# Kernel tuning notes

Hardware: AMD Instinct MI355X
Metric: run time of the kernel (lower is better)

## Reference

```python
import jax, jax.numpy as jnp
import numpy as np

B, S, H = 2, 2048, 2048
NH, NKV = 16, 4
HD = H // NH           # 128
THETA = 1000000.0


def setup_inputs() -> dict:
    key = jax.random.key(0)
    ks = jax.random.split(key, 6)
    s = 0.02
    hidden_states = jax.random.normal(ks[0], (B, S, H), jnp.float32)
    # additive causal mask, broadcast over batch and heads
    causal = jnp.tril(jnp.ones((S, S), bool))
    attention_mask = jnp.where(causal, 0.0, -1e9).astype(jnp.float32)[None, None]
    position_ids = jnp.broadcast_to(jnp.arange(S, dtype=jnp.int32), (B, S))
    wq = jax.random.normal(ks[1], (H, H), jnp.float32) * s
    bq = jnp.zeros((H,), jnp.float32)
    wk = jax.random.normal(ks[2], (H, NKV * HD), jnp.float32) * s
    bk = jnp.zeros((NKV * HD,), jnp.float32)
    wv = jax.random.normal(ks[3], (H, NKV * HD), jnp.float32) * s
    bv = jnp.zeros((NKV * HD,), jnp.float32)
    wo = jax.random.normal(ks[4], (H, H), jnp.float32) * s
    return {"hidden_states": hidden_states, "attention_mask": attention_mask,
            "position_ids": position_ids, "wq": wq, "bq": bq, "wk": wk, "bk": bk,
            "wv": wv, "bv": bv, "wo": wo}


def _rope(x, cos, sin):
    # x: [B,S,h,HD]; interleaved-pair rotation == complex multiply in original
    x2 = x.reshape(*x.shape[:-1], HD // 2, 2)
    x0, x1 = x2[..., 0], x2[..., 1]
    r0 = x0 * cos - x1 * sin
    r1 = x0 * sin + x1 * cos
    return jnp.stack([r0, r1], axis=-1).reshape(x.shape).astype(jnp.float32)


def reference(hidden_states, attention_mask, position_ids, wq, bq, wk, bk, wv, bv, wo):
    bf = jnp.bfloat16
    x = hidden_states.astype(bf)
    # projections in bf16, as flax Dense(dtype=bfloat16)
    q = (x @ wq.astype(bf) + bq.astype(bf)).reshape(B, S, NH, HD)
    k = (x @ wk.astype(bf) + bk.astype(bf)).reshape(B, S, NKV, HD)
    v = (x @ wv.astype(bf) + bv.astype(bf)).reshape(B, S, NKV, HD)
    # RoPE: freqs_cis = exp(1j * pos * inv_freq); real rotation form, identical math
    pos = position_ids[0].astype(jnp.float32)                       # [S]
    inv = 1.0 / (THETA ** (jnp.arange(0, HD, 2, dtype=jnp.float32) / HD))  # [HD/2]
    ang = pos[:, None] * inv[None, :]                               # [S, HD/2]
    cos = jnp.cos(ang)[None, :, None, :]
    sin = jnp.sin(ang)[None, :, None, :]
    q = _rope(q, cos, sin)   # cast to float32 per module dtype
    k = _rope(k, cos, sin)
    cache_k, cache_v = k, v.astype(jnp.float32)
    rep = NH // NKV
    kr = jnp.repeat(k, rep, axis=2)                                 # [B,S,NH,HD]
    vr = jnp.repeat(v, rep, axis=2).astype(jnp.float32)
    scale = 1.0 / np.sqrt(HD).astype(np.float32)
    scores = jnp.einsum('bqhd,bkhd->bhqk', q, kr) * scale + attention_mask
    # float64 cast in original is a no-op w/o x64; softmax runs in float32
    probs = jnp.clip(jax.nn.softmax(scores, axis=-1), 1e-9, 1.0 - 1e-9)
    attn = jnp.einsum('bhqk,bkhd->bqhd', probs, vr).reshape(B, S, H)
    out = attn.astype(bf) @ wo.astype(bf)   # o_proj, no bias, bf16
    return out, (cache_k, cache_v)
```

## Files before the change

kernel.cpp:

```cpp
#include <hip/hip_runtime.h>
#include <hip/hip_bf16.h>
#include <math.h>

#define B_    2
#define S_    2048
#define H_    2048
#define NH_   16
#define NKV_  4
#define HD_   128
#define M_    (B_*S_)
#define NKVH_ (NKV_*HD_)
#define QKVN  3072
#define PSTR  72

typedef __bf16 bf16x8 __attribute__((ext_vector_type(8)));
typedef __bf16 bf16x4 __attribute__((ext_vector_type(4)));
typedef float  f32x4  __attribute__((ext_vector_type(4)));

__device__ __forceinline__ float bf2f(unsigned short u){
  unsigned int i = ((unsigned int)u) << 16; float f;
  __builtin_memcpy(&f, &i, 4); return f;
}
__device__ __forceinline__ unsigned short f2bf(float f){
  unsigned int i; __builtin_memcpy(&i, &f, 4);
  unsigned int r = (i + 0x7fffu + ((i >> 16) & 1u)) >> 16;
  return (unsigned short)r;
}
__device__ __forceinline__ float fast_exp2(float x){
  float r; asm("v_exp_f32 %0, %1" : "=v"(r) : "v"(x)); return r;
}

#define GLOAD_LDS16(g, l) __builtin_amdgcn_global_load_lds( \
    (const __attribute__((address_space(1))) void*)(g), \
    (__attribute__((address_space(3))) void*)(l), 16, 0, 0)

__global__ void k_f32_to_bf16(const float* __restrict__ in, unsigned short* __restrict__ out, int n4){
  int idx = blockIdx.x * blockDim.x + threadIdx.x;
  if (idx >= n4) return;
  float4 v = reinterpret_cast<const float4*>(in)[idx];
  ushort4 o; o.x = f2bf(v.x); o.y = f2bf(v.y); o.z = f2bf(v.z); o.w = f2bf(v.w);
  reinterpret_cast<ushort4*>(out)[idx] = o;
}

__global__ void k_transpose_w(const float* __restrict__ W, unsigned short* __restrict__ Wt, int K, int N){
  __shared__ unsigned short tile[32][36];
  int t = threadIdx.x;
  int k0 = blockIdx.x * 32, n0 = blockIdx.y * 32;
  int kr = t >> 3, nc = (t & 7) * 4;
  float4 v = *reinterpret_cast<const float4*>(&W[(size_t)(k0 + kr) * N + n0 + nc]);
  tile[kr][nc+0] = f2bf(v.x); tile[kr][nc+1] = f2bf(v.y);
  tile[kr][nc+2] = f2bf(v.z); tile[kr][nc+3] = f2bf(v.w);
  __syncthreads();
  int nr = t >> 3, kc = (t & 7) * 4;
  ushort4 o;
  o.x = tile[kc+0][nr]; o.y = tile[kc+1][nr]; o.z = tile[kc+2][nr]; o.w = tile[kc+3][nr];
  *reinterpret_cast<ushort4*>(&Wt[(size_t)(n0 + nr) * K + k0 + kc]) = o;
}

__global__ void k_bias_cat(const float* __restrict__ bq, const float* __restrict__ bk,
                           const float* __restrict__ bv, float* __restrict__ out){
  int i = blockIdx.x * 256 + threadIdx.x;
  if (i >= QKVN) return;
  out[i] = (i < H_) ? bq[i] : (i < H_ + NKVH_ ? bk[i - H_] : bv[i - H_ - NKVH_]);
}

__global__ void k_rope_table(const int* __restrict__ pos, float2* __restrict__ tab){
  int idx = blockIdx.x * blockDim.x + threadIdx.x;
  if (idx >= S_ * 64) return;
  int s = idx >> 6, i = idx & 63;
  float p = (float)pos[s];
  float inv = expf(-(float)i * (13.815510557964274f / 64.0f));
  float ang = p * inv;
  tab[idx] = make_float2(cosf(ang), sinf(ang));
}

__global__ void k_rope_k(unsigned short* __restrict__ QKV, const float2* __restrict__ tab,
                         float* __restrict__ cacheK){
  int idx = blockIdx.x * blockDim.x + threadIdx.x;
  int row = idx >> 7;
  int col0 = (idx & 127) * 4;
  int s = row & (S_ - 1);
  int i0 = (col0 & (HD_ - 1)) >> 1;
  unsigned short* p = QKV + (size_t)row * QKVN + H_ + col0;
  ushort4 v = *reinterpret_cast<ushort4*>(p);
  float2 t0 = tab[(s << 6) + i0], t1 = tab[(s << 6) + i0 + 1];
  float x0 = bf2f(v.x), x1 = bf2f(v.y), x2 = bf2f(v.z), x3 = bf2f(v.w);
  float r0 = x0 * t0.x - x1 * t0.y;
  float r1 = x0 * t0.y + x1 * t0.x;
  float r2 = x2 * t1.x - x3 * t1.y;
  float r3 = x2 * t1.y + x3 * t1.x;
  ushort4 o; o.x = f2bf(r0); o.y = f2bf(r1); o.z = f2bf(r2); o.w = f2bf(r3);
  *reinterpret_cast<ushort4*>(p) = o;
  float4 c; c.x = r0; c.y = r1; c.z = r2; c.w = r3;
  reinterpret_cast<float4*>(cacheK)[idx] = c;
}

__global__ void k_transpose_v(const unsigned short* __restrict__ QKV, unsigned short* __restrict__ Vt,
                              float* __restrict__ cacheV){
  __shared__ unsigned short tile[32][36];
  int t = threadIdx.x;
  int s0 = blockIdx.x * 32, c0 = blockIdx.y * 32, b = blockIdx.z;
  int sr = t >> 3, cc = (t & 7) * 4;
  ushort4 v = *reinterpret_cast<const ushort4*>(
      &QKV[(size_t)(b * S_ + s0 + sr) * QKVN + H_ + NKVH_ + c0 + cc]);
  tile[sr][cc+0] = v.x; tile[sr][cc+1] = v.y; tile[sr][cc+2] = v.z; tile[sr][cc+3] = v.w;
  float4 cf; cf.x = bf2f(v.x); cf.y = bf2f(v.y); cf.z = bf2f(v.z); cf.w = bf2f(v.w);
  *reinterpret_cast<float4*>(&cacheV[(size_t)(b * S_ + s0 + sr) * NKVH_ + c0 + cc]) = cf;
  __syncthreads();
  int cr = t >> 3, sc = (t & 7) * 4;
  ushort4 o;
  o.x = tile[sc+0][cr]; o.y = tile[sc+1][cr]; o.z = tile[sc+2][cr]; o.w = tile[sc+3][cr];
  *reinterpret_cast<ushort4*>(&Vt[(size_t)(b * NKVH_ + c0 + cr) * S_ + s0 + sc]) = o;
}

__global__ __launch_bounds__(256) void k_gemm_bt(
    const unsigned short* __restrict__ A,
    const unsigned short* __restrict__ Bt,
    const float* __restrict__ bias,
    unsigned short* __restrict__ Cb,
    float* __restrict__ Cf,
    int M, int N, int K)
{
  __shared__ unsigned short As[128 * 32];
  __shared__ unsigned short Bs[128 * 32];
  const int nbn = N >> 7;
  const int bm = blockIdx.x / nbn, bn = blockIdx.x % nbn;
  const int tid = threadIdx.x, lane = tid & 63, wave = tid >> 6;
  const int wr = wave >> 1, wc = wave & 1;
  const int gm0 = bm << 7, gn0 = bn << 7;
  const int l15 = lane & 15, lhi = lane >> 4;
  const int srow = lane >> 2, scol = (lane & 3) * 8;

  f32x4 acc[4][4];
  f32x4 zero = {0.f, 0.f, 0.f, 0.f};
  #pragma unroll
  for (int m = 0; m < 4; m++)
    #pragma unroll
    for (int n = 0; n < 4; n++) acc[m][n] = zero;

  for (int k0 = 0; k0 < K; k0 += 32) {
    __syncthreads();
    #pragma unroll
    for (int it = 0; it < 2; ++it) {
      int c = it * 4 + wave;
      const unsigned short* gA = A + (size_t)(gm0 + c * 16 + srow) * K + k0 + scol;
      GLOAD_LDS16(gA, As + c * 512);
      const unsigned short* gB = Bt + (size_t)(gn0 + c * 16 + srow) * K + k0 + scol;
      GLOAD_LDS16(gB, Bs + c * 512);
    }
    __syncthreads();
    bf16x8 af[4], bfr[4];
    #pragma unroll
    for (int m = 0; m < 4; m++)
      af[m] = *reinterpret_cast<const bf16x8*>(&As[(wr * 64 + m * 16 + l15) * 32 + lhi * 8]);
    #pragma unroll
    for (int n = 0; n < 4; n++)
      bfr[n] = *reinterpret_cast<const bf16x8*>(&Bs[(wc * 64 + n * 16 + l15) * 32 + lhi * 8]);
    #pragma unroll
    for (int m = 0; m < 4; m++)
      #pragma unroll
      for (int n = 0; n < 4; n++)
        acc[m][n] = __builtin_amdgcn_mfma_f32_16x16x32_bf16(af[m], bfr[n], acc[m][n], 0, 0, 0);
  }

  #pragma unroll
  for (int m = 0; m < 4; m++) {
    #pragma unroll
    for (int n = 0; n < 4; n++) {
      int col = gn0 + wc * 64 + n * 16 + l15;
      float bv = bias ? bias[col] : 0.0f;
      #pragma unroll
      for (int r = 0; r < 4; r++) {
        int row = gm0 + wr * 64 + m * 16 + lhi * 4 + r;
        size_t idx = (size_t)row * N + col;
        float v = acc[m][n][r] + bv;
        if (Cf) Cf[idx] = bf2f(f2bf(v));
        else    Cb[idx] = f2bf(v);
      }
    }
  }
}

__device__ __forceinline__ bf16x8 rope8(ushort4 a, ushort4 b, const float2* __restrict__ tb, float mul){
  unsigned short u[8];
  float2 c;
  c = tb[0]; { float x0=bf2f(a.x), x1=bf2f(a.y); u[0]=f2bf((x0*c.x-x1*c.y)*mul); u[1]=f2bf((x0*c.y+x1*c.x)*mul); }
  c = tb[1]; { float x0=bf2f(a.z), x1=bf2f(a.w); u[2]=f2bf((x0*c.x-x1*c.y)*mul); u[3]=f2bf((x0*c.y+x1*c.x)*mul); }
  c = tb[2]; { float x0=bf2f(b.x), x1=bf2f(b.y); u[4]=f2bf((x0*c.x-x1*c.y)*mul); u[5]=f2bf((x0*c.y+x1*c.x)*mul); }
  c = tb[3]; { float x0=bf2f(b.z), x1=bf2f(b.w); u[6]=f2bf((x0*c.x-x1*c.y)*mul); u[7]=f2bf((x0*c.y+x1*c.x)*mul); }
  bf16x8 r; __builtin_memcpy(&r, u, 16); return r;
}

__global__ __launch_bounds__(256, 2) void k_attn(
    const unsigned short* __restrict__ QKV,
    const unsigned short* __restrict__ Vt,
    const float2* __restrict__ tab,
    unsigned short* __restrict__ O)
{
  __shared__ unsigned short Ks[2][64 * 128];
  __shared__ unsigned short Vs[128 * 64];
  __shared__ unsigned short Plds[4][32 * PSTR];
  const int qb = blockIdx.x;
  const int h = blockIdx.y, b = blockIdx.z;
  const int tid = threadIdx.x, lane = tid & 63, wave = tid >> 6;
  const int l15 = lane & 15, lhi = lane >> 4;
  const int q0a = qb * 64 + wave * 16;
  const int q0b = (31 - qb) * 64 + wave * 16;
  const int kvh = h >> 2;
  const float scale = 0.08838834764831845f;
  const float LOG2E = 1.4426950408889634f;
  const float SHIFT2 = 23.083120654223414f;

  const unsigned short* Kg = QKV + (size_t)(b * S_) * QKVN + H_ + kvh * HD_;
  const unsigned short* Vg = Vt + (size_t)(b * NKV_ + kvh) * HD_ * S_;

  bf16x8 qfa[4], qfb[4];
  {
    const unsigned short* qa = QKV + (size_t)(b * S_ + q0a + l15) * QKVN + h * HD_ + lhi * 8;
    const unsigned short* qbp = QKV + (size_t)(b * S_ + q0b + l15) * QKVN + h * HD_ + lhi * 8;
    const float2* ta = tab + (size_t)(q0a + l15) * 64;
    const float2* tb = tab + (size_t)(q0b + l15) * 64;
    #pragma unroll
    for (int t = 0; t < 4; t++) {
      int i0 = t * 16 + lhi * 4;
      ushort4 a0 = *reinterpret_cast<const ushort4*>(qa + t * 32);
      ushort4 a1 = *reinterpret_cast<const ushort4*>(qa + t * 32 + 4);
      ushort4 b0 = *reinterpret_cast<const ushort4*>(qbp + t * 32);
      ushort4 b1 = *reinterpret_cast<const ushort4*>(qbp + t * 32 + 4);
      qfa[t] = rope8(a0, a1, ta + i0, scale);
      qfb[t] = rope8(b0, b1, tb + i0, scale);
    }
  }

  f32x4 oa[8], ob[8];
  f32x4 zero = {0.f, 0.f, 0.f, 0.f};
  #pragma unroll
  for (int d = 0; d < 8; d++) { oa[d] = zero; ob[d] = zero; }
  float la = 0.f, lb = 0.f;

  unsigned short* pl = &Plds[wave][0];
  const int ktmax = 31 - qb;
  const int krow = tid >> 4, kch = tid & 15;
  const int vrow = tid >> 3, vch = tid & 7;

  auto STAGE_K = [&](int kt, int bi){
    #pragma unroll
    for (int p = 0; p < 4; p++) {
      int r = p * 16 + krow;
      int cs = kch ^ (r & 7);
      GLOAD_LDS16(Kg + (size_t)(kt * 64 + r) * QKVN + cs * 8, &Ks[bi][(p * 16 + 4 * wave) * 128]);
    }
  };
  auto STAGE_V = [&](int kt){
    #pragma unroll
    for (int p = 0; p < 4; p++) {
      int r = p * 32 + vrow;
      int cs = vch ^ (r & 7);
      GLOAD_LDS16(Vg + (size_t)r * S_ + kt * 64 + cs * 8, &Vs[(p * 32 + 8 * wave) * 64]);
    }
  };

  STAGE_K(0, 0);
  __syncthreads();
  int cur = 0;

  for (int kt = 0; kt <= ktmax; ++kt) {
    STAGE_V(kt);
    if (kt < ktmax) STAGE_K(kt + 1, cur ^ 1);
    const bool doA = (kt <= qb);

    f32x4 sca[4], scb[4];
    #pragma unroll
    for (int c = 0; c < 4; c++) { sca[c] = zero; scb[c] = zero; }
    __builtin_amdgcn_s_setprio(1);
    #pragma unroll
    for (int c = 0; c < 4; c++) {
      int rk = c * 16 + l15;
      #pragma unroll
      for (int t = 0; t < 4; t++) {
        bf16x8 kf = *reinterpret_cast<const bf16x8*>(
            &Ks[cur][rk * 128 + (((t << 2) + lhi) ^ (rk & 7)) * 8]);
        scb[c] = __builtin_amdgcn_mfma_f32_16x16x32_bf16(kf, qfb[t], scb[c], 0, 0, 0);
        if (doA) sca[c] = __builtin_amdgcn_mfma_f32_16x16x32_bf16(kf, qfa[t], sca[c], 0, 0, 0);
      }
    }
    __builtin_amdgcn_s_setprio(0);

    {
      int qiB = q0b + l15;
      float acc = 0.f;
      #pragma unroll
      for (int c = 0; c < 4; c++) {
        float pv[4];
        #pragma unroll
        for (int r = 0; r < 4; r++) {
          int key = kt * 64 + c * 16 + lhi * 4 + r;
          float sv = (key > qiB) ? -1e30f : scb[c][r];
          pv[r] = fast_exp2(fmaf(sv, LOG2E, -SHIFT2));
          acc += pv[r];
        }
        bf16x4 w;
        w[0] = (__bf16)pv[0]; w[1] = (__bf16)pv[1]; w[2] = (__bf16)pv[2]; w[3] = (__bf16)pv[3];
        *reinterpret_cast<bf16x4*>(&pl[(16 + l15) * PSTR + c * 16 + lhi * 4]) = w;
      }
      lb += acc;
    }
    if (doA) {
      int qiA = q0a + l15;
      float acc = 0.f;
      #pragma unroll
      for (int c = 0; c < 4; c++) {
        float pv[4];
        #pragma unroll
        for (int r = 0; r < 4; r++) {
          int key = kt * 64 + c * 16 + lhi * 4 + r;
          float sv = (key > qiA) ? -1e30f : sca[c][r];
          pv[r] = fast_exp2(fmaf(sv, LOG2E, -SHIFT2));
          acc += pv[r];
        }
        bf16x4 w;
        w[0] = (__bf16)pv[0]; w[1] = (__bf16)pv[1]; w[2] = (__bf16)pv[2]; w[3] = (__bf16)pv[3];
        *reinterpret_cast<bf16x4*>(&pl[l15 * PSTR + c * 16 + lhi * 4]) = w;
      }
      la += acc;
    }
    asm volatile("" ::: "memory");
    bf16x8 pfb0 = *reinterpret_cast<const bf16x8*>(&pl[(16 + l15) * PSTR + lhi * 8]);
    bf16x8 pfb1 = *reinterpret_cast<const bf16x8*>(&pl[(16 + l15) * PSTR + 32 + lhi * 8]);
    bf16x8 pfa0 = pfb0, pfa1 = pfb1;
    if (doA) {
      pfa0 = *reinterpret_cast<const bf16x8*>(&pl[l15 * PSTR + lhi * 8]);
      pfa1 = *reinterpret_cast<const bf16x8*>(&pl[l15 * PSTR + 32 + lhi * 8]);
    }
    asm volatile("" ::: "memory");

    __syncthreads();

    __builtin_amdgcn_s_setprio(1);
    #pragma unroll
    for (int d = 0; d < 8; d++) {
      int rv = d * 16 + l15;
      bf16x8 vf0 = *reinterpret_cast<const bf16x8*>(&Vs[rv * 64 + (lhi ^ (rv & 7)) * 8]);
      bf16x8 vf1 = *reinterpret_cast<const bf16x8*>(&Vs[rv * 64 + ((4 + lhi) ^ (rv & 7)) * 8]);
      ob[d] = __builtin_amdgcn_mfma_f32_16x16x32_bf16(pfb0, vf0, ob[d], 0, 0, 0);
      ob[d] = __builtin_amdgcn_mfma_f32_16x16x32_bf16(pfb1, vf1, ob[d], 0, 0, 0);
      if (doA) {
        oa[d] = __builtin_amdgcn_mfma_f32_16x16x32_bf16(pfa0, vf0, oa[d], 0, 0, 0);
        oa[d] = __builtin_amdgcn_mfma_f32_16x16x32_bf16(pfa1, vf1, oa[d], 0, 0, 0);
      }
    }
    __builtin_amdgcn_s_setprio(0);

    __syncthreads();
    cur ^= 1;
  }

  la += __shfl_xor(la, 16); la += __shfl_xor(la, 32);
  lb += __shfl_xor(lb, 16); lb += __shfl_xor(lb, 32);

  #pragma unroll
  for (int r = 0; r < 4; r++) {
    int src = (lane & 48) | (lhi * 4 + r);
    float invA = 1.0f / __shfl(la, src);
    float invB = 1.0f / __shfl(lb, src);
    size_t offA = (size_t)(b * S_ + q0a + lhi * 4 + r) * H_ + h * HD_;
    size_t offB = (size_t)(b * S_ + q0b + lhi * 4 + r) * H_ + h * HD_;
    #pragma unroll
    for (int d = 0; d < 8; d++) {
      O[offA + d * 16 + l15] = f2bf(oa[d][r] * invA);
      O[offB + d * 16 + l15] = f2bf(ob[d][r] * invB);
    }
  }
}

extern "C" void kernel_launch(void* const* d_in, const int* in_sizes, int n_in,
                              void* d_out, int out_size, void* d_ws, size_t ws_size,
                              hipStream_t stream) {
  const float* hidden = (const float*)d_in[0];
  const int*   pos    = (const int*)d_in[2];
  const float* wq     = (const float*)d_in[3];
  const float* bq     = (const float*)d_in[4];
  const float* wk     = (const float*)d_in[5];
  const float* bk     = (const float*)d_in[6];
  const float* wv     = (const float*)d_in[7];
  const float* bv     = (const float*)d_in[8];
  const float* wo     = (const float*)d_in[9];

  float* outF   = (float*)d_out;
  float* cacheK = outF + (size_t)M_ * H_;
  float* cacheV = cacheK + (size_t)M_ * NKVH_;

  char* w = (char*)d_ws;
  unsigned short* Xbf  = (unsigned short*)w; w += (size_t)M_ * H_ * 2;
  unsigned short* WqT  = (unsigned short*)w; w += (size_t)H_ * H_ * 2;
  unsigned short* WkT  = (unsigned short*)w; w += (size_t)NKVH_ * H_ * 2;
  unsigned short* WvT  = (unsigned short*)w; w += (size_t)NKVH_ * H_ * 2;
  unsigned short* WoT  = (unsigned short*)w; w += (size_t)H_ * H_ * 2;
  unsigned short* QKVw = (unsigned short*)w; w += (size_t)M_ * QKVN * 2;
  unsigned short* Vt   = (unsigned short*)w; w += (size_t)M_ * NKVH_ * 2;
  float2*         tab  = (float2*)w;         w += (size_t)S_ * 64 * sizeof(float2);
  float*       biasQKV = (float*)w;          w += QKVN * sizeof(float);
  unsigned short* Ao   = Xbf;

  k_f32_to_bf16<<<(M_ * H_ / 4) / 256, 256, 0, stream>>>(hidden, Xbf, M_ * H_ / 4);
  k_transpose_w<<<dim3(64, 64), 256, 0, stream>>>(wq, WqT, H_, H_);
  k_transpose_w<<<dim3(64, 16), 256, 0, stream>>>(wk, WkT, H_, NKVH_);
  k_transpose_w<<<dim3(64, 16), 256, 0, stream>>>(wv, WvT, H_, NKVH_);
  k_transpose_w<<<dim3(64, 64), 256, 0, stream>>>(wo, WoT, H_, H_);
  k_rope_table<<<(S_ * 64) / 256, 256, 0, stream>>>(pos, tab);
  k_bias_cat<<<(QKVN + 255) / 256, 256, 0, stream>>>(bq, bk, bv, biasQKV);
  k_gemm_bt<<<32 * (QKVN >> 7), 256, 0, stream>>>(Xbf, WqT, biasQKV, QKVw, nullptr, M_, QKVN, H_);
  k_rope_k<<<(M_ * NKVH_ / 4) / 256, 256, 0, stream>>>(QKVw, tab, cacheK);
  k_transpose_v<<<dim3(S_ / 32, NKVH_ / 32, B_), 256, 0, stream>>>(QKVw, Vt, cacheV);
  k_attn<<<dim3(16, NH_, B_), 256, 0, stream>>>(QKVw, Vt, tab, Ao);
  k_gemm_bt<<<32 * 16, 256, 0, stream>>>(Ao, WoT, nullptr, nullptr, outF, M_, H_, H_);
}
```

Before: 241.5 us.

## Rewrite projection GEMM with 256x256 tiles, double-buffered LDS and swizzle

Replaces the 128x128, K=32 GEMM with a 512-thread 256x256 tile kernel using K=64 steps. Global-to-LDS loads for the next K tile are double-buffered and interleaved with the MFMA work. The LDS layout is XOR-swizzled to avoid bank conflicts, and blocks are remapped across XCDs. The aim is higher arithmetic intensity and overlap of loads with compute in both projection GEMMs. The costs are 128KB of LDS and 128 accumulator registers per thread, which limit occupancy, and fewer workgroups (192 and 128), which may underfill the 256 CUs.

```diff
diff --git a/kernel.cpp b/kernel.cpp
--- a/kernel.cpp
+++ b/kernel.cpp
@@ -113,7 +113,7 @@
   *reinterpret_cast<ushort4*>(&Vt[(size_t)(b * NKVH_ + c0 + cr) * S_ + s0 + sc]) = o;
 }
 
-__global__ __launch_bounds__(256) void k_gemm_bt(
+__global__ __launch_bounds__(512, 2) void k_gemm256(
     const unsigned short* __restrict__ A,
     const unsigned short* __restrict__ Bt,
     const float* __restrict__ bias,
@@ -121,59 +121,92 @@
     float* __restrict__ Cf,
     int M, int N, int K)
 {
-  __shared__ unsigned short As[128 * 32];
-  __shared__ unsigned short Bs[128 * 32];
-  const int nbn = N >> 7;
-  const int bm = blockIdx.x / nbn, bn = blockIdx.x % nbn;
+  __shared__ unsigned short As[2][256 * 64];
+  __shared__ unsigned short Bs[2][256 * 64];
+  const int nbn = N >> 8;
+  const int nwg = gridDim.x;
+  int bid = blockIdx.x;
+  if ((nwg & 7) == 0) bid = (bid & 7) * (nwg >> 3) + (bid >> 3);
+  const int bm = bid / nbn, bn = bid % nbn;
   const int tid = threadIdx.x, lane = tid & 63, wave = tid >> 6;
-  const int wr = wave >> 1, wc = wave & 1;
-  const int gm0 = bm << 7, gn0 = bn << 7;
+  const int wm = wave >> 2, wn = wave & 3;
+  const int gm0 = bm << 8, gn0 = bn << 8;
   const int l15 = lane & 15, lhi = lane >> 4;
-  const int srow = lane >> 2, scol = (lane & 3) * 8;
-
-  f32x4 acc[4][4];
+  const int srow = lane >> 3;
+  const int sch  = (lane & 7) ^ srow;
+
+  f32x4 acc[8][4];
   f32x4 zero = {0.f, 0.f, 0.f, 0.f};
   #pragma unroll
-  for (int m = 0; m < 4; m++)
+  for (int m = 0; m < 8; m++)
     #pragma unroll
     for (int n = 0; n < 4; n++) acc[m][n] = zero;
 
-  for (int k0 = 0; k0 < K; k0 += 32) {
+  const int nt = K >> 6;
+
+  auto STAGE_P = [&](int kt, int bi, int p){
+    int row = p * 64 + wave * 8 + srow;
+    GLOAD_LDS16(A  + (size_t)(gm0 + row) * K + kt * 64 + sch * 8,
+                &As[bi][(p * 64 + wave * 8) * 64]);
+    GLOAD_LDS16(Bt + (size_t)(gn0 + row) * K + kt * 64 + sch * 8,
+                &Bs[bi][(p * 64 + wave * 8) * 64]);
+  };
+
+  #pragma unroll
+  for (int p = 0; p < 4; p++) STAGE_P(0, 0, p);
+  __syncthreads();
+
+  for (int kt = 0; kt < nt; ++kt) {
+    const int cur = kt & 1, nxt = cur ^ 1;
+    const bool pre = (kt + 1 < nt);
+
+    bf16x8 bfr[4][2];
+    #pragma unroll
+    for (int nf = 0; nf < 4; nf++) {
+      int row = wn * 64 + nf * 16 + l15;
+      #pragma unroll
+      for (int kk = 0; kk < 2; kk++)
+        bfr[nf][kk] = *reinterpret_cast<const bf16x8*>(
+            &Bs[cur][row * 64 + (((kk << 2) + lhi) ^ (row & 7)) * 8]);
+    }
+
+    #pragma unroll
+    for (int pp = 0; pp < 4; pp++) {
+      if (pre) STAGE_P(kt + 1, nxt, pp);
+      bf16x8 af[2][2];
+      #pragma unroll
+      for (int m2 = 0; m2 < 2; m2++) {
+        int row = wm * 128 + (pp * 2 + m2) * 16 + l15;
+        #pragma unroll
+        for (int kk = 0; kk < 2; kk++)
+          af[m2][kk] = *reinterpret_cast<const bf16x8*>(
+              &As[cur][row * 64 + (((kk << 2) + lhi) ^ (row & 7)) * 8]);
+      }
+      __builtin_amdgcn_s_setprio(1);
+      #pragma unroll
+      for (int m2 = 0; m2 < 2; m2++)
+        #pragma unroll
+        for (int nf = 0; nf < 4; nf++)
+          #pragma unroll
+          for (int kk = 0; kk < 2; kk++)
+            acc[pp * 2 + m2][nf] = __builtin_amdgcn_mfma_f32_16x16x32_bf16(
+                af[m2][kk], bfr[nf][kk], acc[pp * 2 + m2][nf], 0, 0, 0);
+      __builtin_amdgcn_s_setprio(0);
+    }
     __syncthreads();
-    #pragma unroll
-    for (int it = 0; it < 2; ++it) {
-      int c = it * 4 + wave;
-      const unsigned short* gA = A + (size_t)(gm0 + c * 16 + srow) * K + k0 + scol;
-      GLOAD_LDS16(gA, As + c * 512);
-      const unsigned short* gB = Bt + (size_t)(gn0 + c * 16 + srow) * K + k0 + scol;
-      GLOAD_LDS16(gB, Bs + c * 512);
-    }
-    __syncthreads();
-    bf16x8 af[4], bfr[4];
-    #pragma unroll
-    for (int m = 0; m < 4; m++)
-      af[m] = *reinterpret_cast<const bf16x8*>(&As[(wr * 64 + m * 16 + l15) * 32 + lhi * 8]);
-    #pragma unroll
-    for (int n = 0; n < 4; n++)
-      bfr[n] = *reinterpret_cast<const bf16x8*>(&Bs[(wc * 64 + n * 16 + l15) * 32 + lhi * 8]);
-    #pragma unroll
-    for (int m = 0; m < 4; m++)
-      #pragma unroll
-      for (int n = 0; n < 4; n++)
-        acc[m][n] = __builtin_amdgcn_mfma_f32_16x16x32_bf16(af[m], bfr[n], acc[m][n], 0, 0, 0);
   }
 
   #pragma unroll
-  for (int m = 0; m < 4; m++) {
-    #pragma unroll
-    for (int n = 0; n < 4; n++) {
-      int col = gn0 + wc * 64 + n * 16 + l15;
+  for (int mf = 0; mf < 8; mf++) {
+    #pragma unroll
+    for (int nf = 0; nf < 4; nf++) {
+      int col = gn0 + wn * 64 + nf * 16 + l15;
       float bv = bias ? bias[col] : 0.0f;
       #pragma unroll
       for (int r = 0; r < 4; r++) {
-        int row = gm0 + wr * 64 + m * 16 + lhi * 4 + r;
+        int row = gm0 + wm * 128 + mf * 16 + lhi * 4 + r;
         size_t idx = (size_t)row * N + col;
-        float v = acc[m][n][r] + bv;
+        float v = acc[mf][nf][r] + bv;
         if (Cf) Cf[idx] = bf2f(f2bf(v));
         else    Cb[idx] = f2bf(v);
       }
@@ -409,9 +442,9 @@
   k_transpose_w<<<dim3(64, 64), 256, 0, stream>>>(wo, WoT, H_, H_);
   k_rope_table<<<(S_ * 64) / 256, 256, 0, stream>>>(pos, tab);
   k_bias_cat<<<(QKVN + 255) / 256, 256, 0, stream>>>(bq, bk, bv, biasQKV);
-  k_gemm_bt<<<32 * (QKVN >> 7), 256, 0, stream>>>(Xbf, WqT, biasQKV, QKVw, nullptr, M_, QKVN, H_);
+  k_gemm256<<<(M_ >> 8) * (QKVN >> 8), 512, 0, stream>>>(Xbf, WqT, biasQKV, QKVw, nullptr, M_, QKVN, H_);
   k_rope_k<<<(M_ * NKVH_ / 4) / 256, 256, 0, stream>>>(QKVw, tab, cacheK);
   k_transpose_v<<<dim3(S_ / 32, NKVH_ / 32, B_), 256, 0, stream>>>(QKVw, Vt, cacheV);
   k_attn<<<dim3(16, NH_, B_), 256, 0, stream>>>(QKVw, Vt, tab, Ao);
-  k_gemm_bt<<<32 * 16, 256, 0, stream>>>(Ao, WoT, nullptr, nullptr, outF, M_, H_, H_);
-}
+  k_gemm256<<<(M_ >> 8) * (H_ >> 8), 512, 0, stream>>>(Ao, WoT, nullptr, nullptr, outF, M_, H_, H_);
+}
```

New measurement: 229.1 us. -5.2%, faster.
